# Performance work log

Measured on AMD Instinct MI355X. Metric: run time of the kernel, lower is better.

Reference implementation:

```python
import jax, jax.numpy as jnp
import numpy as np

D_MODEL = 1024
N_HEADS = 16
D_HEAD = D_MODEL // N_HEADS
B, S = 2, 2048


def setup_inputs() -> dict:
    key = jax.random.key(0)
    ks = jax.random.split(key, 8)
    scale = 1.0 / np.sqrt(D_MODEL)
    return {
        "x": jax.random.normal(ks[0], (B, S, D_MODEL), dtype=jnp.float32),
        "Wq": jax.random.normal(ks[1], (D_MODEL, D_MODEL), dtype=jnp.float32) * scale,
        "bq": jnp.zeros((D_MODEL,), dtype=jnp.float32),
        "Wk": jax.random.normal(ks[2], (D_MODEL, D_MODEL), dtype=jnp.float32) * scale,
        "bk": jnp.zeros((D_MODEL,), dtype=jnp.float32),
        "Wv": jax.random.normal(ks[3], (D_MODEL, D_MODEL), dtype=jnp.float32) * scale,
        "bv": jnp.zeros((D_MODEL,), dtype=jnp.float32),
        "Wo": jax.random.normal(ks[4], (D_MODEL, D_MODEL), dtype=jnp.float32) * scale,
    }


def reference(x, Wq, bq, Wk, bk, Wv, bv, Wo):
    Bsz, Slen, D = x.shape
    # projections -> [B, H, S, Dh]
    def split_heads(t):
        return t.reshape(Bsz, Slen, N_HEADS, D_HEAD).transpose(0, 2, 1, 3)
    q = split_heads(x @ Wq + bq)
    k = split_heads(x @ Wk + bk)
    v = split_heads(x @ Wv + bv)
    scale = jnp.sqrt(jnp.float32(D_HEAD))
    scores = jnp.einsum('bhsd,bhtd->bhst', q, k) / scale  # [B,H,S,S]
    causal_mask = jnp.tril(jnp.ones((Slen, Slen), dtype=jnp.bool_))
    scores = jnp.where(causal_mask, scores, jnp.finfo(scores.dtype).min)
    attn = jax.nn.softmax(scores, axis=-1)
    # deterministic=True path: dropout is identity
    out = jnp.einsum('bhst,bhtd->bhsd', attn, v)
    out = out.transpose(0, 2, 1, 3).reshape(Bsz, Slen, D)
    return out @ Wo
```

## Files before the change

kernel.cpp:

```cpp
#include <hip/hip_runtime.h>
#include <hip/hip_bf16.h>

#define BATCH   2
#define SEQ     2048
#define DMODEL  1024
#define NHEADS  16
#define DHEAD   64
#define MROWS   (BATCH*SEQ)
#define NBH     (BATCH*NHEADS)

typedef float  f32x4  __attribute__((ext_vector_type(4)));
typedef short  s16x4  __attribute__((ext_vector_type(4)));
typedef short  s16x8  __attribute__((ext_vector_type(8)));
typedef __bf16 bf16x8 __attribute__((ext_vector_type(8)));

__device__ __forceinline__ short f2bf(float f) {
  union { float f; unsigned u; } v; v.f = f;
  return (short)((v.u + 0x7fffu + ((v.u >> 16) & 1u)) >> 16);
}
__device__ __forceinline__ float bf2f(short s) {
  union { unsigned u; float f; } v; v.u = ((unsigned)(unsigned short)s) << 16;
  return v.f;
}

__global__ void convert_x(const float* __restrict__ x, short* __restrict__ xb) {
  int i = (blockIdx.x * 256 + threadIdx.x) * 4;
  float4 v = *(const float4*)(x + i);
  s16x4 o = { f2bf(v.x), f2bf(v.y), f2bf(v.z), f2bf(v.w) };
  *(s16x4*)(xb + i) = o;
}

__global__ void transpose_w(const float* __restrict__ Wq, const float* __restrict__ Wk,
                            const float* __restrict__ Wv, const float* __restrict__ Wo,
                            short* __restrict__ WtQKV, short* __restrict__ WtO) {
  __shared__ float t[32][33];
  const float* W; short* Wt;
  int z = blockIdx.z;
  if      (z == 0) { W = Wq; Wt = WtQKV; }
  else if (z == 1) { W = Wk; Wt = WtQKV + (1u << 20); }
  else if (z == 2) { W = Wv; Wt = WtQKV + (2u << 20); }
  else             { W = Wo; Wt = WtO; }
  int n0 = blockIdx.x * 32, k0 = blockIdx.y * 32;
  int tx = threadIdx.x, ty = threadIdx.y;
  #pragma unroll
  for (int i = 0; i < 32; i += 8) t[ty + i][tx] = W[(k0 + ty + i) * DMODEL + n0 + tx];
  __syncthreads();
  #pragma unroll
  for (int i = 0; i < 32; i += 8) Wt[(n0 + ty + i) * DMODEL + k0 + tx] = f2bf(t[tx][ty + i]);
}

template<int MT, int NT, int EPI>
__global__ __launch_bounds__(256) void gemm_bf16(
    const short* __restrict__ A, const short* __restrict__ Bt,
    const float* __restrict__ bq, const float* __restrict__ bk, const float* __restrict__ bv,
    short* __restrict__ qb, short* __restrict__ kb, short* __restrict__ vt,
    float* __restrict__ out)
{
  constexpr int K = DMODEL, BK = 32;
  constexpr int WM = MT / 2, WN = NT / 2;
  constexpr int TM = WM / 16, TN = WN / 16;
  constexpr int CA = MT * BK / 512;
  constexpr int CB = NT * BK / 512;
  constexpr int TP = 136;
  constexpr int SME = (EPI == 0) ? 128 * TP : (MT * BK + NT * BK);
  __shared__ short smem[SME];
  short* la = smem;
  short* lb = smem + MT * BK;
  const int tid = threadIdx.x;
  const int wave = tid >> 6, lane = tid & 63;
  const int quad = lane >> 4, l16 = lane & 15;
  const int wr = wave >> 1, wc = wave & 1;
  const int m0 = blockIdx.y * MT, n0 = blockIdx.x * NT;
  const int arow = lane >> 2, acol = (lane & 3) * 8;

  f32x4 acc[TM][TN] = {};

  for (int k0 = 0; k0 < K; k0 += BK) {
    for (int c = wave; c < CA; c += 4) {
      const short* gp = A + (m0 + c * 16 + arow) * K + k0 + acol;
      __builtin_amdgcn_global_load_lds((__attribute__((address_space(1))) void*)gp,
                                       (__attribute__((address_space(3))) void*)(la + c * 512),
                                       16, 0, 0);
    }
    for (int c = wave; c < CB; c += 4) {
      const short* gp = Bt + (n0 + c * 16 + arow) * K + k0 + acol;
      __builtin_amdgcn_global_load_lds((__attribute__((address_space(1))) void*)gp,
                                       (__attribute__((address_space(3))) void*)(lb + c * 512),
                                       16, 0, 0);
    }
    __syncthreads();
    bf16x8 af[TM], bfr[TN];
    #pragma unroll
    for (int i = 0; i < TM; ++i)
      af[i] = *(const bf16x8*)&la[(wr * WM + i * 16 + l16) * BK + quad * 8];
    #pragma unroll
    for (int j = 0; j < TN; ++j)
      bfr[j] = *(const bf16x8*)&lb[(wc * WN + j * 16 + l16) * BK + quad * 8];
    #pragma unroll
    for (int i = 0; i < TM; ++i)
      #pragma unroll
      for (int j = 0; j < TN; ++j)
        acc[i][j] = __builtin_amdgcn_mfma_f32_16x16x32_bf16(af[i], bfr[j], acc[i][j], 0, 0, 0);
    __syncthreads();
  }

  if constexpr (EPI == 0) {
    const bool isV = (n0 >= 2 * DMODEL);
    const float* bias; int nbase; float scl;
    if (n0 < DMODEL)          { bias = bq; nbase = 0;          scl = 0.125f * 1.44269504089f; }
    else if (n0 < 2 * DMODEL) { bias = bk; nbase = DMODEL;     scl = 1.f; }
    else                      { bias = bv; nbase = 2 * DMODEL; scl = 1.f; }
    #pragma unroll
    for (int j = 0; j < TN; ++j) {
      int coll = wc * WN + j * 16 + l16;
      float bias_v = bias[n0 - nbase + coll];
      #pragma unroll
      for (int i = 0; i < TM; ++i) {
        int rowl = wr * WM + i * 16 + quad * 4;
        #pragma unroll
        for (int r = 0; r < 4; ++r) {
          short v = f2bf((acc[i][j][r] + bias_v) * scl);
          if (isV) smem[coll * TP + rowl + r] = v;
          else     smem[(rowl + r) * TP + coll] = v;
        }
      }
    }
    __syncthreads();
    const int b = m0 >> 11, s0 = m0 & (SEQ - 1);
    const int rseg = tid & 15, rrow = tid >> 4;
    if (!isV) {
      short* dst = (n0 < DMODEL) ? qb : kb;
      #pragma unroll
      for (int it = 0; it < 8; ++it) {
        int row = it * 16 + rrow;
        int colg = (n0 - nbase) + rseg * 8;
        int h = colg >> 6, d = colg & 63;
        s16x8 v = *(const s16x8*)&smem[row * TP + rseg * 8];
        *(s16x8*)(dst + ((b * NHEADS + h) * SEQ + s0 + row) * DHEAD + d) = v;
      }
    } else {
      #pragma unroll
      for (int it = 0; it < 8; ++it) {
        int drow = it * 16 + rrow;
        int colg = (n0 - nbase) + drow;
        int h = colg >> 6, d = colg & 63;
        s16x8 v = *(const s16x8*)&smem[drow * TP + rseg * 8];
        *(s16x8*)(vt + ((b * NHEADS + h) * DHEAD + d) * SEQ + s0 + rseg * 8) = v;
      }
    }
  } else {
    #pragma unroll
    for (int i = 0; i < TM; ++i)
      #pragma unroll
      for (int r = 0; r < 4; ++r) {
        int mrow = m0 + wr * WM + i * 16 + quad * 4 + r;
        #pragma unroll
        for (int j = 0; j < TN; ++j)
          out[mrow * DMODEL + n0 + wc * WN + j * 16 + l16] = acc[i][j][r];
      }
    (void)bq; (void)bk; (void)bv; (void)qb; (void)kb; (void)vt;
  }
}


__global__ __launch_bounds__(256, 2) void attn_k(
    const short* __restrict__ qbp, const short* __restrict__ kbp,
    const short* __restrict__ vtb, short* __restrict__ oP, float* __restrict__ lP)
{
  __shared__ short kls[2][4096];
  __shared__ short vls[2][4096];
  const int tid = threadIdx.x, wave = tid >> 6, lane = tid & 63;
  const int quad = lane >> 4, l16 = lane & 15;
  const int half = blockIdx.x & 1;
  const int bh = (blockIdx.x >> 1) & 31;
  const int qg = blockIdx.x >> 6;
  const int qt1 = qg * 8 + wave * 2;
  const int mF[4] = { qt1 * 16, (qt1 + 1) * 16, (126 - qt1) * 16, (127 - qt1) * 16 };
  const int nch = (127 - 8 * qg) / 4 + 1;
  const short* Q  = qbp + bh * SEQ * DHEAD;
  const short* Kp = kbp + bh * SEQ * DHEAD;
  const short* Vt = vtb + bh * DHEAD * SEQ;

  bf16x8 qf[4][2];
  #pragma unroll
  for (int f = 0; f < 4; ++f) {
    qf[f][0] = *(const bf16x8*)&Q[(mF[f] + l16) * DHEAD + quad * 8];
    qf[f][1] = *(const bf16x8*)&Q[(mF[f] + l16) * DHEAD + 32 + quad * 8];
  }

  float lF[4] = {};
  f32x4 oF[4][4] = {};

  const int vdl = lane >> 3, vsl = lane & 7;

  auto stage = [&](int buf, int t0) {
    #pragma unroll
    for (int j = 0; j < 2; ++j) {
      int g = j * 4 + wave;
      const short* gp = Kp + (t0 + lane) * DHEAD + g * 8;
      __builtin_amdgcn_global_load_lds((__attribute__((address_space(1))) void*)gp,
                                       (__attribute__((address_space(3))) void*)&kls[buf][g * 512],
                                       16, 0, 0);
    }
    #pragma unroll
    for (int j = 0; j < 2; ++j) {
      int gd = j * 4 + wave;
      const short* gp = Vt + (gd * 8 + vdl) * SEQ + t0 + ((vsl ^ vdl) * 8);
      __builtin_amdgcn_global_load_lds((__attribute__((address_space(1))) void*)gp,
                                       (__attribute__((address_space(3))) void*)&vls[buf][gd * 512],
                                       16, 0, 0);
    }
  };

  stage(0, half * 64);
  for (int c = half; c < nch; c += 2) {
    __syncthreads();
    if (c + 2 < nch) stage(((c >> 1) + 1) & 1, (c + 2) * 64);
    const int t0 = c * 64;
    const int buf = (c >> 1) & 1;
    #pragma unroll
    for (int t = 0; t < 4; ++t) {
      const int tb = t0 + t * 16;
      if (tb <= mF[3]) {
        bf16x8 kf0 = *(const bf16x8*)&kls[buf][((0 + quad) * 64 + t * 16 + l16) * 8];
        bf16x8 kf1 = *(const bf16x8*)&kls[buf][((4 + quad) * 64 + t * 16 + l16) * 8];
        s16x4 vf[4];
        {
          int gsw = ((t * 2 + (quad >> 1)) ^ (l16 & 7));
          #pragma unroll
          for (int dt = 0; dt < 4; ++dt)
            vf[dt] = *(const s16x4*)&vls[buf][((dt * 16 + l16) * 8 + gsw) * 8 + (quad & 1) * 4];
        }
        #pragma unroll
        for (int f = 0; f < 4; ++f) {
          if (tb <= mF[f]) {
            f32x4 a = {};
            a = __builtin_amdgcn_mfma_f32_16x16x32_bf16(kf0, qf[f][0], a, 0, 0, 0);
            a = __builtin_amdgcn_mfma_f32_16x16x32_bf16(kf1, qf[f][1], a, 0, 0, 0);
            if (tb == mF[f]) {
              #pragma unroll
              for (int r = 0; r < 4; ++r)
                if (quad * 4 + r > l16) a[r] = -1e30f;
            }
            f32x4 p;
            #pragma unroll
            for (int r = 0; r < 4; ++r) p[r] = __builtin_amdgcn_exp2f(a[r]);
            lF[f] += (p[0] + p[1]) + (p[2] + p[3]);
            __hip_bfloat162 c01 = __float22bfloat162_rn(float2{p[0], p[1]});
            __hip_bfloat162 c23 = __float22bfloat162_rn(float2{p[2], p[3]});
            union { unsigned u[2]; s16x4 s; } pu;
            pu.u[0] = *(unsigned*)&c01; pu.u[1] = *(unsigned*)&c23;
            #pragma unroll
            for (int dt = 0; dt < 4; ++dt)
              oF[f][dt] = __builtin_amdgcn_mfma_f32_16x16x16bf16_1k(pu.s, vf[dt], oF[f][dt], 0, 0, 0);
          }
        }
      }
    }
  }

  float* lD = lP + (half * NBH + bh) * SEQ;
  short* oD = oP + ((half * NBH + bh) * SEQ) * DHEAD;
  #pragma unroll
  for (int f = 0; f < 4; ++f) {
    float l = lF[f];
    l += __shfl_xor(l, 16, 64); l += __shfl_xor(l, 32, 64);
    if (quad == 0) lD[mF[f] + l16] = l;
    #pragma unroll
    for (int r = 0; r < 4; ++r) {
      int s = mF[f] + quad * 4 + r;
      #pragma unroll
      for (int dt = 0; dt < 4; ++dt)
        oD[s * DHEAD + dt * 16 + l16] = f2bf(oF[f][dt][r]);
    }
  }
}

__global__ void attn_merge(const short* __restrict__ oP, const float* __restrict__ lP,
                           short* __restrict__ ob) {
  int idx = blockIdx.x * 256 + threadIdx.x;
  int d8 = idx & 7, s = (idx >> 3) & (SEQ - 1), bh = idx >> 14;
  s16x8 e = *(const s16x8*)&oP[((0   + bh) * SEQ + s) * DHEAD + d8 * 8];
  s16x8 o = *(const s16x8*)&oP[((NBH + bh) * SEQ + s) * DHEAD + d8 * 8];
  float linv = 1.0f / (lP[bh * SEQ + s] + lP[(NBH + bh) * SEQ + s]);
  s16x8 r;
  #pragma unroll
  for (int k = 0; k < 8; ++k) r[k] = f2bf((bf2f(e[k]) + bf2f(o[k])) * linv);
  int b = bh >> 4, h = bh & 15;
  *(s16x8*)&ob[(b * SEQ + s) * DMODEL + h * DHEAD + d8 * 8] = r;
}

extern "C" void kernel_launch(void* const* d_in, const int* in_sizes, int n_in,
                              void* d_out, int out_size, void* d_ws, size_t ws_size,
                              hipStream_t stream) {
  const float* x  = (const float*)d_in[0];
  const float* Wq = (const float*)d_in[1];
  const float* bq = (const float*)d_in[2];
  const float* Wk = (const float*)d_in[3];
  const float* bk = (const float*)d_in[4];
  const float* Wv = (const float*)d_in[5];
  const float* bv = (const float*)d_in[6];
  const float* Wo = (const float*)d_in[7];
  float* out = (float*)d_out;

  char* ws = (char*)d_ws;
  short* xb  = (short*)(ws);
  short* wtq = (short*)(ws + (8u  << 20));
  short* oP  = (short*)(ws);
  short* qb  = (short*)(ws + (16u << 20));
  short* kb  = (short*)(ws + (24u << 20));
  short* vt  = (short*)(ws + (32u << 20));
  short* ob  = (short*)(ws + (40u << 20));
  short* wto = (short*)(ws + (48u << 20));
  float* lP  = (float*)(ws + (50u << 20));

  convert_x<<<MROWS * DMODEL / 1024, 256, 0, stream>>>(x, xb);
  transpose_w<<<dim3(32, 32, 4), dim3(32, 8), 0, stream>>>(Wq, Wk, Wv, Wo, wtq, wto);

  gemm_bf16<128, 128, 0><<<dim3(3 * DMODEL / 128, MROWS / 128), 256, 0, stream>>>(
      xb, wtq, bq, bk, bv, qb, kb, vt, nullptr);

  attn_k<<<NBH * 8 * 2, 256, 0, stream>>>(qb, kb, vt, oP, lP);
  attn_merge<<<NBH * SEQ * 8 / 256, 256, 0, stream>>>(oP, lP, ob);

  gemm_bf16<64, 128, 1><<<dim3(DMODEL / 128, MROWS / 64), 256, 0, stream>>>(
      ob, wto, nullptr, nullptr, nullptr, nullptr, nullptr, nullptr, out);
}
```

Measured before the change: 192.9 us.

## Fuse prep kernels, deepen GEMM K-tile, stage two KV chunks per attention step

Merges the x conversion and weight transpose into a single launch, which saves one kernel launch. Doubles the GEMM K tile from 32 to 64 so there are half as many barrier iterations, at the cost of more LDS per block. The attention kernel now stages two 64-key chunks per barrier, doubling its K/V LDS buffers, and the workspace layout is moved to avoid the oP aliasing xb. The larger LDS footprint in both kernels may reduce occupancy.

After: 206.5 us. +7.0%, slower.

```diff
diff --git a/kernel.cpp b/kernel.cpp
--- a/kernel.cpp
+++ b/kernel.cpp
@@ -23,25 +23,27 @@
   return v.f;
 }
 
-__global__ void convert_x(const float* __restrict__ x, short* __restrict__ xb) {
-  int i = (blockIdx.x * 256 + threadIdx.x) * 4;
-  float4 v = *(const float4*)(x + i);
-  s16x4 o = { f2bf(v.x), f2bf(v.y), f2bf(v.z), f2bf(v.w) };
-  *(s16x4*)(xb + i) = o;
-}
-
-__global__ void transpose_w(const float* __restrict__ Wq, const float* __restrict__ Wk,
-                            const float* __restrict__ Wv, const float* __restrict__ Wo,
-                            short* __restrict__ WtQKV, short* __restrict__ WtO) {
+__global__ void prep_fused(const float* __restrict__ x, short* __restrict__ xb,
+                           const float* __restrict__ Wq, const float* __restrict__ Wk,
+                           const float* __restrict__ Wv, const float* __restrict__ Wo,
+                           short* __restrict__ WtQKV, short* __restrict__ WtO) {
   __shared__ float t[32][33];
+  int z = blockIdx.z;
+  int tx = threadIdx.x, ty = threadIdx.y;
+  if (z >= 4) {
+    int blk = (z - 4) * 1024 + blockIdx.y * 32 + blockIdx.x;
+    int i = (blk * 256 + ty * 32 + tx) * 4;
+    float4 v = *(const float4*)(x + i);
+    s16x4 o = { f2bf(v.x), f2bf(v.y), f2bf(v.z), f2bf(v.w) };
+    *(s16x4*)(xb + i) = o;
+    return;
+  }
   const float* W; short* Wt;
-  int z = blockIdx.z;
   if      (z == 0) { W = Wq; Wt = WtQKV; }
   else if (z == 1) { W = Wk; Wt = WtQKV + (1u << 20); }
   else if (z == 2) { W = Wv; Wt = WtQKV + (2u << 20); }
   else             { W = Wo; Wt = WtO; }
   int n0 = blockIdx.x * 32, k0 = blockIdx.y * 32;
-  int tx = threadIdx.x, ty = threadIdx.y;
   #pragma unroll
   for (int i = 0; i < 32; i += 8) t[ty + i][tx] = W[(k0 + ty + i) * DMODEL + n0 + tx];
   __syncthreads();
@@ -56,13 +58,14 @@
     short* __restrict__ qb, short* __restrict__ kb, short* __restrict__ vt,
     float* __restrict__ out)
 {
-  constexpr int K = DMODEL, BK = 32;
+  constexpr int K = DMODEL, BK = 64;
   constexpr int WM = MT / 2, WN = NT / 2;
   constexpr int TM = WM / 16, TN = WN / 16;
   constexpr int CA = MT * BK / 512;
   constexpr int CB = NT * BK / 512;
   constexpr int TP = 136;
-  constexpr int SME = (EPI == 0) ? 128 * TP : (MT * BK + NT * BK);
+  constexpr int STG = (MT + NT) * BK;
+  constexpr int SME = (EPI == 0) ? (STG > 128 * TP ? STG : 128 * TP) : STG;
   __shared__ short smem[SME];
   short* la = smem;
   short* lb = smem + MT * BK;
@@ -71,36 +74,42 @@
   const int quad = lane >> 4, l16 = lane & 15;
   const int wr = wave >> 1, wc = wave & 1;
   const int m0 = blockIdx.y * MT, n0 = blockIdx.x * NT;
-  const int arow = lane >> 2, acol = (lane & 3) * 8;
+  const int arow = lane >> 3, acol = (lane & 7) * 8;
 
   f32x4 acc[TM][TN] = {};
 
   for (int k0 = 0; k0 < K; k0 += BK) {
     for (int c = wave; c < CA; c += 4) {
-      const short* gp = A + (m0 + c * 16 + arow) * K + k0 + acol;
+      const short* gp = A + (m0 + c * 8 + arow) * K + k0 + acol;
       __builtin_amdgcn_global_load_lds((__attribute__((address_space(1))) void*)gp,
                                        (__attribute__((address_space(3))) void*)(la + c * 512),
                                        16, 0, 0);
     }
     for (int c = wave; c < CB; c += 4) {
-      const short* gp = Bt + (n0 + c * 16 + arow) * K + k0 + acol;
+      const short* gp = Bt + (n0 + c * 8 + arow) * K + k0 + acol;
       __builtin_amdgcn_global_load_lds((__attribute__((address_space(1))) void*)gp,
                                        (__attribute__((address_space(3))) void*)(lb + c * 512),
                                        16, 0, 0);
     }
     __syncthreads();
-    bf16x8 af[TM], bfr[TN];
+    bf16x8 af[TM][2], bfr[TN][2];
     #pragma unroll
     for (int i = 0; i < TM; ++i)
-      af[i] = *(const bf16x8*)&la[(wr * WM + i * 16 + l16) * BK + quad * 8];
+      #pragma unroll
+      for (int h = 0; h < 2; ++h)
+        af[i][h] = *(const bf16x8*)&la[(wr * WM + i * 16 + l16) * BK + h * 32 + quad * 8];
     #pragma unroll
     for (int j = 0; j < TN; ++j)
-      bfr[j] = *(const bf16x8*)&lb[(wc * WN + j * 16 + l16) * BK + quad * 8];
+      #pragma unroll
+      for (int h = 0; h < 2; ++h)
+        bfr[j][h] = *(const bf16x8*)&lb[(wc * WN + j * 16 + l16) * BK + h * 32 + quad * 8];
     #pragma unroll
     for (int i = 0; i < TM; ++i)
       #pragma unroll
-      for (int j = 0; j < TN; ++j)
-        acc[i][j] = __builtin_amdgcn_mfma_f32_16x16x32_bf16(af[i], bfr[j], acc[i][j], 0, 0, 0);
+      for (int j = 0; j < TN; ++j) {
+        acc[i][j] = __builtin_amdgcn_mfma_f32_16x16x32_bf16(af[i][0], bfr[j][0], acc[i][j], 0, 0, 0);
+        acc[i][j] = __builtin_amdgcn_mfma_f32_16x16x32_bf16(af[i][1], bfr[j][1], acc[i][j], 0, 0, 0);
+      }
     __syncthreads();
   }
 
@@ -167,8 +176,8 @@
     const short* __restrict__ qbp, const short* __restrict__ kbp,
     const short* __restrict__ vtb, short* __restrict__ oP, float* __restrict__ lP)
 {
-  __shared__ short kls[2][4096];
-  __shared__ short vls[2][4096];
+  __shared__ short kls[2][8192];
+  __shared__ short vls[2][8192];
   const int tid = threadIdx.x, wave = tid >> 6, lane = tid & 63;
   const int quad = lane >> 4, l16 = lane & 15;
   const int half = blockIdx.x & 1;
@@ -193,13 +202,13 @@
 
   const int vdl = lane >> 3, vsl = lane & 7;
 
-  auto stage = [&](int buf, int t0) {
+  auto stage1 = [&](int buf, int slot, int t0) {
     #pragma unroll
     for (int j = 0; j < 2; ++j) {
       int g = j * 4 + wave;
       const short* gp = Kp + (t0 + lane) * DHEAD + g * 8;
       __builtin_amdgcn_global_load_lds((__attribute__((address_space(1))) void*)gp,
-                                       (__attribute__((address_space(3))) void*)&kls[buf][g * 512],
+                                       (__attribute__((address_space(3))) void*)&kls[buf][slot * 4096 + g * 512],
                                        16, 0, 0);
     }
     #pragma unroll
@@ -207,52 +216,64 @@
       int gd = j * 4 + wave;
       const short* gp = Vt + (gd * 8 + vdl) * SEQ + t0 + ((vsl ^ vdl) * 8);
       __builtin_amdgcn_global_load_lds((__attribute__((address_space(1))) void*)gp,
-                                       (__attribute__((address_space(3))) void*)&vls[buf][gd * 512],
+                                       (__attribute__((address_space(3))) void*)&vls[buf][slot * 4096 + gd * 512],
                                        16, 0, 0);
     }
   };
-
-  stage(0, half * 64);
-  for (int c = half; c < nch; c += 2) {
+  auto stagepair = [&](int buf, int cc) {
+    stage1(buf, 0, cc * 64);
+    if (cc + 2 < nch) stage1(buf, 1, (cc + 2) * 64);
+  };
+
+  stagepair(0, half);
+  int it = 0;
+  for (int cc = half; cc < nch; cc += 4, ++it) {
     __syncthreads();
-    if (c + 2 < nch) stage(((c >> 1) + 1) & 1, (c + 2) * 64);
-    const int t0 = c * 64;
-    const int buf = (c >> 1) & 1;
-    #pragma unroll
-    for (int t = 0; t < 4; ++t) {
-      const int tb = t0 + t * 16;
-      if (tb <= mF[3]) {
-        bf16x8 kf0 = *(const bf16x8*)&kls[buf][((0 + quad) * 64 + t * 16 + l16) * 8];
-        bf16x8 kf1 = *(const bf16x8*)&kls[buf][((4 + quad) * 64 + t * 16 + l16) * 8];
-        s16x4 vf[4];
-        {
-          int gsw = ((t * 2 + (quad >> 1)) ^ (l16 & 7));
-          #pragma unroll
-          for (int dt = 0; dt < 4; ++dt)
-            vf[dt] = *(const s16x4*)&vls[buf][((dt * 16 + l16) * 8 + gsw) * 8 + (quad & 1) * 4];
-        }
+    if (cc + 4 < nch) stagepair((it + 1) & 1, cc + 4);
+    const int buf = it & 1;
+    #pragma unroll
+    for (int u = 0; u < 2; ++u) {
+      const int c = cc + 2 * u;
+      if (c < nch) {
+        const int t0 = c * 64;
+        const int sb = u * 4096;
         #pragma unroll
-        for (int f = 0; f < 4; ++f) {
-          if (tb <= mF[f]) {
-            f32x4 a = {};
-            a = __builtin_amdgcn_mfma_f32_16x16x32_bf16(kf0, qf[f][0], a, 0, 0, 0);
-            a = __builtin_amdgcn_mfma_f32_16x16x32_bf16(kf1, qf[f][1], a, 0, 0, 0);
-            if (tb == mF[f]) {
+        for (int t = 0; t < 4; ++t) {
+          const int tb = t0 + t * 16;
+          if (tb <= mF[3]) {
+            bf16x8 kf0 = *(const bf16x8*)&kls[buf][sb + ((0 + quad) * 64 + t * 16 + l16) * 8];
+            bf16x8 kf1 = *(const bf16x8*)&kls[buf][sb + ((4 + quad) * 64 + t * 16 + l16) * 8];
+            s16x4 vf[4];
+            {
+              int gsw = ((t * 2 + (quad >> 1)) ^ (l16 & 7));
               #pragma unroll
-              for (int r = 0; r < 4; ++r)
-                if (quad * 4 + r > l16) a[r] = -1e30f;
+              for (int dt = 0; dt < 4; ++dt)
+                vf[dt] = *(const s16x4*)&vls[buf][sb + ((dt * 16 + l16) * 8 + gsw) * 8 + (quad & 1) * 4];
             }
-            f32x4 p;
             #pragma unroll
-            for (int r = 0; r < 4; ++r) p[r] = __builtin_amdgcn_exp2f(a[r]);
-            lF[f] += (p[0] + p[1]) + (p[2] + p[3]);
-            __hip_bfloat162 c01 = __float22bfloat162_rn(float2{p[0], p[1]});
-            __hip_bfloat162 c23 = __float22bfloat162_rn(float2{p[2], p[3]});
-            union { unsigned u[2]; s16x4 s; } pu;
-            pu.u[0] = *(unsigned*)&c01; pu.u[1] = *(unsigned*)&c23;
-            #pragma unroll
-            for (int dt = 0; dt < 4; ++dt)
-              oF[f][dt] = __builtin_amdgcn_mfma_f32_16x16x16bf16_1k(pu.s, vf[dt], oF[f][dt], 0, 0, 0);
+            for (int f = 0; f < 4; ++f) {
+              if (tb <= mF[f]) {
+                f32x4 a = {};
+                a = __builtin_amdgcn_mfma_f32_16x16x32_bf16(kf0, qf[f][0], a, 0, 0, 0);
+                a = __builtin_amdgcn_mfma_f32_16x16x32_bf16(kf1, qf[f][1], a, 0, 0, 0);
+                if (tb == mF[f]) {
+                  #pragma unroll
+                  for (int r = 0; r < 4; ++r)
+                    if (quad * 4 + r > l16) a[r] = -1e30f;
+                }
+                f32x4 p;
+                #pragma unroll
+                for (int r = 0; r < 4; ++r) p[r] = __builtin_amdgcn_exp2f(a[r]);
+                lF[f] += (p[0] + p[1]) + (p[2] + p[3]);
+                __hip_bfloat162 c01 = __float22bfloat162_rn(float2{p[0], p[1]});
+                __hip_bfloat162 c23 = __float22bfloat162_rn(float2{p[2], p[3]});
+                union { unsigned u2[2]; s16x4 s; } pu;
+                pu.u2[0] = *(unsigned*)&c01; pu.u2[1] = *(unsigned*)&c23;
+                #pragma unroll
+                for (int dt = 0; dt < 4; ++dt)
+                  oF[f][dt] = __builtin_amdgcn_mfma_f32_16x16x16bf16_1k(pu.s, vf[dt], oF[f][dt], 0, 0, 0);
+              }
+            }
           }
         }
       }
@@ -306,21 +327,20 @@
   char* ws = (char*)d_ws;
   short* xb  = (short*)(ws);
   short* wtq = (short*)(ws + (8u  << 20));
-  short* oP  = (short*)(ws);
+  short* wto = (short*)(ws + (14u << 20));
   short* qb  = (short*)(ws + (16u << 20));
   short* kb  = (short*)(ws + (24u << 20));
   short* vt  = (short*)(ws + (32u << 20));
   short* ob  = (short*)(ws + (40u << 20));
-  short* wto = (short*)(ws + (48u << 20));
-  float* lP  = (float*)(ws + (50u << 20));
-
-  convert_x<<<MROWS * DMODEL / 1024, 256, 0, stream>>>(x, xb);
-  transpose_w<<<dim3(32, 32, 4), dim3(32, 8), 0, stream>>>(Wq, Wk, Wv, Wo, wtq, wto);
+  short* oP  = (short*)(ws + (48u << 20));
+  float* lP  = (float*)(ws + (80u << 20));
+
+  prep_fused<<<dim3(32, 32, 8), dim3(32, 8), 0, stream>>>(x, xb, Wq, Wk, Wv, Wo, wtq, wto);
 
   gemm_bf16<128, 128, 0><<<dim3(3 * DMODEL / 128, MROWS / 128), 256, 0, stream>>>(
       xb, wtq, bq, bk, bv, qb, kb, vt, nullptr);
 
-  attn_k<<<NBH * 8 * 2, 256, 0, stream>>>(qb, kb, vt, oP, lP);
+  attn_k<<<8 * NBH * 2, 256, 0, stream>>>(qb, kb, vt, oP, lP);
   attn_merge<<<NBH * SEQ * 8 / 256, 256, 0, stream>>>(oP, lP, ob);
 
   gemm_bf16<64, 128, 1><<<dim3(DMODEL / 128, MROWS / 64), 256, 0, stream>>>(
```
